# Performance work log

Hardware: AMD Instinct MI355X
Metric: run time of the kernel (lower is better)

The kernel has to match this reference:

```python
import jax, jax.numpy as jnp
import numpy as np

N, E, R = 30000, 300000, 3
IN, HID, OUT, HEADS = 256, 32, 64, 4
NEG_SLOPE = 0.2  # DGL GATConv default


def setup_inputs() -> dict:
    key = jax.random.key(0)
    ks = jax.random.split(key, 10)
    x = jax.random.normal(ks[0], (N, IN), jnp.float32)
    src = jax.random.randint(ks[1], (R, E), 0, N)
    dst = jax.random.randint(ks[2], (R, E), 0, N)
    s1 = (2.0 / IN) ** 0.5
    W1 = jax.random.normal(ks[3], (R, IN, HEADS * HID), jnp.float32) * s1
    attn_l1 = jax.random.normal(ks[4], (R, HEADS, HID), jnp.float32) * 0.1
    attn_r1 = jax.random.normal(ks[5], (R, HEADS, HID), jnp.float32) * 0.1
    b1 = jnp.zeros((R, HEADS * HID), jnp.float32)
    s2 = (2.0 / (HEADS * HID)) ** 0.5
    W2 = jax.random.normal(ks[6], (R, HEADS * HID, HEADS * OUT), jnp.float32) * s2
    attn_l2 = jax.random.normal(ks[7], (R, HEADS, OUT), jnp.float32) * 0.1
    attn_r2 = jax.random.normal(ks[8], (R, HEADS, OUT), jnp.float32) * 0.1
    b2 = jnp.zeros((R, HEADS * OUT), jnp.float32)
    return dict(x=x, src=src, dst=dst, W1=W1, attn_l1=attn_l1, attn_r1=attn_r1,
                b1=b1, W2=W2, attn_l2=attn_l2, attn_r2=attn_r2, b2=b2)


def _gat(x, s, d, W, al, ar, b):
    """Single-relation GATConv (DGL semantics): gather, edge softmax, scatter."""
    n = x.shape[0]
    H, D = al.shape
    z = (x @ W).reshape(n, H, D)                 # [n,H,D]
    el = (z * al[None]).sum(-1)                  # [n,H]
    er = (z * ar[None]).sum(-1)                  # [n,H]
    e = jax.nn.leaky_relu(el[s] + er[d], NEG_SLOPE)   # [E,H]
    m = jax.ops.segment_max(e, d, num_segments=n)     # stable edge softmax per dst
    w = jnp.exp(e - m[d])
    denom = jax.ops.segment_sum(w, d, num_segments=n)
    alpha = w / denom[d]                         # [E,H]
    out = jax.ops.segment_sum(alpha[:, :, None] * z[s], d, num_segments=n)  # [n,H,D]
    return out + b.reshape(1, H, D)


def reference(x, src, dst, W1, attn_l1, attn_r1, b1, W2, attn_l2, attn_r2, b2):
    gat_r = jax.vmap(_gat, in_axes=(None, 0, 0, 0, 0, 0, 0))
    # conv1: per-relation GAT summed across relations (HeteroGraphConv aggregate='sum')
    h = gat_r(x, src, dst, W1, attn_l1, attn_r1, b1).sum(0)      # [N,HEADS,HID]
    h = jax.nn.relu(h).reshape(-1, HEADS * HID)                  # [N,HEADS*HID]
    # conv2
    h2 = gat_r(h, src, dst, W2, attn_l2, attn_r2, b2).sum(0)     # [N,HEADS,OUT]
    return h2.mean(axis=1)                                       # [N,OUT]
```

## Files before the change

kernel.cpp:

```cpp
#include <hip/hip_runtime.h>
#include <math.h>

#define NNODES 30000
#define MPAD   30080
#define NEDGES 300000
#define NREL 3
#define IND 256
#define HIDD 32
#define OUTD 64
#define NHEADS 4
#define C1 (NHEADS*HIDD)
#define C2 (NHEADS*OUTD)
#define NEG_SLOPE 0.2f
#define CAP 64

typedef short bf16x8 __attribute__((ext_vector_type(8)));
typedef float f32x4  __attribute__((ext_vector_type(4)));
typedef float f32x2  __attribute__((ext_vector_type(2)));

__device__ __forceinline__ float b2f(unsigned short u) {
    return __uint_as_float(((unsigned)u) << 16);
}
__device__ __forceinline__ unsigned short f2b(float f) {
    unsigned u = __float_as_uint(f);
    u += 0x7fffu + ((u >> 16) & 1u);
    return (unsigned short)(u >> 16);
}

template<int CTRL>
__device__ __forceinline__ float dppadd(float x) {
    int s = __builtin_amdgcn_update_dpp(0, __float_as_int(x), CTRL, 0xf, 0xf, true);
    return x + __int_as_float(s);
}
__device__ __forceinline__ float dpp_wsum63(float x) {
    x = dppadd<0x111>(x);
    x = dppadd<0x112>(x);
    x = dppadd<0x114>(x);
    x = dppadd<0x118>(x);
    x = dppadd<0x142>(x);
    x = dppadd<0x143>(x);
    return x;
}
__device__ __forceinline__ float wave_rcp_sum(float w) {
    float den = __uint_as_float(__builtin_amdgcn_readlane(
        __float_as_uint(dpp_wsum63(w)), 63));
    return __builtin_amdgcn_rcpf(den);
}

template<int K, int N>
__device__ __forceinline__ void pack_w_dev(const float* __restrict__ W,
                                           unsigned short* __restrict__ P, int t) {
    const int KS = K / 32, NT = N / 16;
    int lane = t & 63;
    int fid = t >> 6;
    if (fid >= NREL * NT * KS) return;
    int ks = fid % KS;
    int nt = (fid / KS) % NT;
    int r  = fid / (KS * NT);
    int n  = nt * 16 + (lane & 15);
    int k0 = ks * 32 + (lane >> 4) * 8;
    const float* Wr = W + (size_t)r * K * N;
    unsigned short o[8];
#pragma unroll
    for (int j = 0; j < 8; j++) o[j] = f2b(Wr[(size_t)(k0 + j) * N + n]);
    unsigned short* dst = P + (size_t)fid * 512 + lane * 8;
    *(ushort4*)&dst[0] = *(ushort4*)&o[0];
    *(ushort4*)&dst[4] = *(ushort4*)&o[4];
}

__device__ __forceinline__ void pack_v_dev(const float* __restrict__ W2,
                                           unsigned short* __restrict__ P, int t) {
    const int KS = 16, NT = 4;
    int lane = t & 63;
    int fid = t >> 6;
    if (fid >= NREL * NT * KS) return;
    int ks = fid % KS;
    int nt = (fid / KS) % NT;
    int r  = fid / (KS * NT);
    int n  = nt * 16 + (lane & 15);
    int k0 = ks * 32 + (lane >> 4) * 8;
    const float* Wr = W2 + (size_t)r * C1 * C2;
    unsigned short o[8];
#pragma unroll
    for (int j = 0; j < 8; j++) {
        int k = k0 + j;
        int c = k & 127, h = k >> 7;
        o[j] = f2b(Wr[(size_t)c * C2 + h * OUTD + n]);
    }
    unsigned short* dst = P + (size_t)fid * 512 + lane * 8;
    *(ushort4*)&dst[0] = *(ushort4*)&o[0];
    *(ushort4*)&dst[4] = *(ushort4*)&o[4];
}

#define BF_BLOCKS ((NREL * NEDGES + 255) / 256)
#define PACK1_BLOCKS (NREL * (C1/16) * (IND/32) / 4)
#define PACKV_BLOCKS (NREL * 4 * 16 / 4)
#define VLR_BLOCKS 6
#define PREP_BLOCKS (BF_BLOCKS + PACK1_BLOCKS + PACKV_BLOCKS + VLR_BLOCKS + 1)
__global__ void prep_kernel(const int* __restrict__ src, const int* __restrict__ dst,
                            unsigned* __restrict__ cnt, int* __restrict__ buck,
                            const float* __restrict__ W1, unsigned short* __restrict__ P1,
                            const float* __restrict__ W2, unsigned short* __restrict__ PV,
                            const float* __restrict__ al2, const float* __restrict__ ar2,
                            const float* __restrict__ bb2,
                            float* __restrict__ tabs, float* __restrict__ biasout) {
    int b = blockIdx.x;
    if (b < BF_BLOCKS) {
        int gid = b * 256 + threadIdx.x;
        if (gid >= NREL * NEDGES) return;
        int r = gid / NEDGES;
        int d = dst[gid];
        int base = r * NNODES + d;
        unsigned pos = atomicAdd(&cnt[base], 1u);
        if (pos < CAP) buck[(size_t)base * CAP + pos] = src[gid];
    } else if (b < BF_BLOCKS + PACK1_BLOCKS) {
        pack_w_dev<IND, C1>(W1, P1, (b - BF_BLOCKS) * 256 + threadIdx.x);
    } else if (b < BF_BLOCKS + PACK1_BLOCKS + PACKV_BLOCKS) {
        pack_v_dev(W2, PV, (b - BF_BLOCKS - PACK1_BLOCKS) * 256 + threadIdx.x);
    } else if (b < BF_BLOCKS + PACK1_BLOCKS + PACKV_BLOCKS + VLR_BLOCKS) {
        int t = (b - BF_BLOCKS - PACK1_BLOCKS - PACKV_BLOCKS) * 256 + threadIdx.x;
        if (t < NREL * NHEADS * C1) {
            int c = t & 127, rh = t >> 7;
            const float* Wr = W2 + (size_t)(rh >> 2) * C1 * C2 + (size_t)c * C2 + (rh & 3) * OUTD;
            const float* alp = al2 + (size_t)rh * OUTD;
            const float* arp = ar2 + (size_t)rh * OUTD;
            float sl = 0.f, sr = 0.f;
#pragma unroll 4
            for (int d = 0; d < OUTD; d++) {
                sl = fmaf(Wr[d], alp[d], sl);
                sr = fmaf(Wr[d], arp[d], sr);
            }
            tabs[(rh * 2 + 0) * C1 + c] = sl;
            tabs[(rh * 2 + 1) * C1 + c] = sr;
        }
    } else {
        int t = threadIdx.x;
        if (t < OUTD) {
            float s = 0.f;
#pragma unroll
            for (int rh = 0; rh < NREL * NHEADS; rh++)
                s += bb2[(size_t)(rh >> 2) * C2 + (rh & 3) * OUTD + t];
            biasout[t] = 0.25f * s;
        }
    }
}

template<int K, int N>
__global__ __launch_bounds__(256) void mfma_gemm(
    const float* __restrict__ Ax, const unsigned short* __restrict__ Bp,
    const float* __restrict__ al, const float* __restrict__ ar,
    unsigned short* __restrict__ Zh, float* __restrict__ el, float* __restrict__ er)
{
    const int KS = K / 32, NT = N / 16, MT = 64, NP = N + 4;
    const int wave = threadIdx.x >> 6, lane = threadIdx.x & 63;
    const int r  = blockIdx.y;
    const int m0 = blockIdx.x * MT;
    const int fcol = lane & 15, quad = lane >> 4;

    __shared__ unsigned short zs[MT * (N + 4)];

    int m = m0 + wave * 16 + fcol;
    if (m >= NNODES) m = NNODES - 1;
    bf16x8 afrag[KS];
    const float* arowp = Ax + (size_t)m * K + quad * 8;
#pragma unroll
    for (int ks = 0; ks < KS; ks++) {
        float4 fa = *(const float4*)(arowp + ks * 32);
        float4 fb = *(const float4*)(arowp + ks * 32 + 4);
        unsigned short t[8] = { f2b(fa.x), f2b(fa.y), f2b(fa.z), f2b(fa.w),
                                f2b(fb.x), f2b(fb.y), f2b(fb.z), f2b(fb.w) };
        afrag[ks] = *(const bf16x8*)t;
    }

    f32x4 acc[NT];
#pragma unroll
    for (int nt = 0; nt < NT; nt++) { f32x4 z = {0.f,0.f,0.f,0.f}; acc[nt] = z; }

    const unsigned short* Bpr = Bp + (size_t)r * NT * KS * 512;
    for (int ks = 0; ks < KS; ks++) {
        bf16x8 b[NT];
#pragma unroll
        for (int nt = 0; nt < NT; nt++)
            b[nt] = *(const bf16x8*)(Bpr + ((size_t)nt * KS + ks) * 512 + lane * 8);
#pragma unroll
        for (int nt = 0; nt < NT; nt++)
            acc[nt] = __builtin_amdgcn_mfma_f32_16x16x32_bf16(afrag[ks], b[nt], acc[nt], 0, 0, 0);
    }

    {
        int lrow = wave * 16 + quad * 4;
#pragma unroll
        for (int nt = 0; nt < NT; nt++)
#pragma unroll
            for (int q = 0; q < 4; q++)
                zs[(lrow + q) * NP + nt * 16 + fcol] = f2b(acc[nt][q]);
    }
    __syncthreads();

    {
        uint2* zo = (uint2*)(Zh + ((size_t)r * MPAD + m0) * N);
        for (int i = threadIdx.x; i < MT * N / 4; i += 256) {
            int row = i / (N / 4), c4 = i % (N / 4);
            zo[i] = *(const uint2*)&zs[row * NP + c4 * 4];
        }
    }
    {
        const int D = N / NHEADS;
        int row = threadIdx.x >> 2, h = threadIdx.x & 3;
        int n = m0 + row;
        if (n < NNODES) {
            const float* alp = al + ((size_t)r * NHEADS + h) * D;
            const float* arp = ar + ((size_t)r * NHEADS + h) * D;
            const unsigned short* zp = zs + row * NP + h * D;
            float sl = 0.f, sr = 0.f;
#pragma unroll
            for (int d0 = 0; d0 < D; d0 += 4) {
                uint2 u = *(const uint2*)&zp[d0];
                float z0 = b2f((unsigned short)(u.x & 0xffff));
                float z1 = b2f((unsigned short)(u.x >> 16));
                float z2 = b2f((unsigned short)(u.y & 0xffff));
                float z3 = b2f((unsigned short)(u.y >> 16));
                sl = fmaf(z0, alp[d0], sl);     sr = fmaf(z0, arp[d0], sr);
                sl = fmaf(z1, alp[d0 + 1], sl); sr = fmaf(z1, arp[d0 + 1], sr);
                sl = fmaf(z2, alp[d0 + 2], sl); sr = fmaf(z2, arp[d0 + 2], sr);
                sl = fmaf(z3, alp[d0 + 3], sl); sr = fmaf(z3, arp[d0 + 3], sr);
            }
            el[((size_t)r * NNODES + n) * NHEADS + h] = sl;
            er[((size_t)r * NNODES + n) * NHEADS + h] = sr;
        }
    }
}

__global__ __launch_bounds__(256) void gat_gather1(
    const unsigned* __restrict__ cnt, const int* __restrict__ buck,
    const float* __restrict__ el, const float* __restrict__ er,
    const unsigned short* __restrict__ Zh, const float* __restrict__ b1,
    const float* __restrict__ tabs,
    unsigned short* __restrict__ hbh, float* __restrict__ el2, float* __restrict__ er2)
{
    __shared__ float atab[4][4 * 65];
    int wave = threadIdx.x >> 6, lane = threadIdx.x & 63;
    int n = blockIdx.x * 4 + wave;
    const int h0 = lane >> 4;
    float accx = 0.f, accy = 0.f;
    for (int r = 0; r < NREL; r++) {
        int base = r * NNODES + n;
        int c = (int)cnt[base]; c = c < CAP ? c : CAP;
        if (c == 0) continue;
        int s_all = buck[(size_t)base * CAP + (lane < c ? lane : c - 1)];
        float lg[4];
        if (lane < c) {
            const float4 e4 = *(const float4*)&el[((size_t)r * NNODES + s_all) * NHEADS];
            const float4 r4 = *(const float4*)&er[(size_t)base * NHEADS];
            float v;
            v = e4.x + r4.x; lg[0] = v > 0.f ? v : NEG_SLOPE * v;
            v = e4.y + r4.y; lg[1] = v > 0.f ? v : NEG_SLOPE * v;
            v = e4.z + r4.z; lg[2] = v > 0.f ? v : NEG_SLOPE * v;
            v = e4.w + r4.w; lg[3] = v > 0.f ? v : NEG_SLOPE * v;
        } else {
            lg[0] = lg[1] = lg[2] = lg[3] = -INFINITY;
        }
#pragma unroll
        for (int h = 0; h < 4; h++) {
            float w = __expf(lg[h]);
            float rinv = wave_rcp_sum(w);
            atab[wave][h * 65 + lane] = w * rinv;
        }
        const unsigned short* Zr = Zh + (size_t)r * MPAD * C1;
        const float* at = atab[wave] + h0 * 65;
        int cc = (c + 7) & ~7;
        for (int j = 0; j < cc; j += 8) {
            int ss[8];
#pragma unroll
            for (int q = 0; q < 8; q++) ss[q] = __builtin_amdgcn_readlane(s_all, j + q);
            unsigned zz[8];
#pragma unroll
            for (int q = 0; q < 8; q++)
                zz[q] = *(const unsigned*)&Zr[(size_t)ss[q] * C1 + 2 * lane];
#pragma unroll
            for (int q = 0; q < 8; q++) {
                float a0 = at[j + q];
                float z0 = __uint_as_float(zz[q] << 16);
                float z1 = __uint_as_float(zz[q] & 0xffff0000u);
                accx = fmaf(a0, z0, accx);
                accy = fmaf(a0, z1, accy);
            }
        }
    }
    int cch = 2 * lane;
    float bx = b1[cch]     + b1[C1 + cch]     + b1[2 * C1 + cch];
    float by = b1[cch + 1] + b1[C1 + cch + 1] + b1[2 * C1 + cch + 1];
    ushort2 o;
    o.x = f2b(fmaxf(accx + bx, 0.f));
    o.y = f2b(fmaxf(accy + by, 0.f));
    *(ushort2*)&hbh[(size_t)n * C1 + cch] = o;

    float hx = b2f(o.x), hy = b2f(o.y);
    for (int half = 0; half < 2; half++) {
        float p[12];
#pragma unroll
        for (int j = 0; j < 12; j++) {
            const float2 t = *(const float2*)&tabs[(half * 12 + j) * C1 + cch];
            p[j] = fmaf(hy, t.y, hx * t.x);
        }
#pragma unroll
        for (int j = 0; j < 12; j++) p[j] = dpp_wsum63(p[j]);
        if (lane == 63) {
#pragma unroll
            for (int j = 0; j < 12; j++) {
                int jj = half * 12 + j;
                int rh = jj >> 1;
                size_t idx = ((size_t)(rh >> 2) * NNODES + n) * NHEADS + (rh & 3);
                if (jj & 1) er2[idx] = p[j]; else el2[idx] = p[j];
            }
        }
    }
}

__global__ __launch_bounds__(512, 8) void gat_gather2f(
    const unsigned* __restrict__ cnt, const int* __restrict__ buck,
    const float* __restrict__ el, const float* __restrict__ er,
    const unsigned short* __restrict__ hbh, const unsigned short* __restrict__ PV,
    const float* __restrict__ biasout, float* __restrict__ out)
{
    __shared__ unsigned short aggs[8 * 1536];
    __shared__ float atv[8][64 * 4];
    const int wave = threadIdx.x >> 6, lane = threadIdx.x & 63;
    const int fcol = lane & 15, quad = lane >> 4;
    const int n0 = blockIdx.x * 8;
    const int n  = n0 + wave;

    for (int r = 0; r < NREL; r++) {
        f32x2 ag0 = {0.f, 0.f}, ag1 = {0.f, 0.f}, ag2 = {0.f, 0.f}, ag3 = {0.f, 0.f};

        int base = r * NNODES + n;
        int c = (int)cnt[base]; c = c < CAP ? c : CAP;
        if (c > 0) {
            int s_all = buck[(size_t)base * CAP + (lane < c ? lane : c - 1)];
            float lg[4];
            if (lane < c) {
                const float4 e4 = *(const float4*)&el[((size_t)r * NNODES + s_all) * NHEADS];
                const float4 r4 = *(const float4*)&er[(size_t)base * NHEADS];
                float v;
                v = e4.x + r4.x; lg[0] = v > 0.f ? v : NEG_SLOPE * v;
                v = e4.y + r4.y; lg[1] = v > 0.f ? v : NEG_SLOPE * v;
                v = e4.z + r4.z; lg[2] = v > 0.f ? v : NEG_SLOPE * v;
                v = e4.w + r4.w; lg[3] = v > 0.f ? v : NEG_SLOPE * v;
            } else {
                lg[0] = lg[1] = lg[2] = lg[3] = -INFINITY;
            }
            float aw[4];
#pragma unroll
            for (int h = 0; h < 4; h++) {
                float w = __expf(lg[h]);
                aw[h] = w * wave_rcp_sum(w);
            }
            float4 aq = { aw[0], aw[1], aw[2], aw[3] };
            *(float4*)&atv[wave][lane * 4] = aq;
            const float* at4 = &atv[wave][0];

            int cc = (c + 7) & ~7;
            for (int j = 0; j < cc; j += 8) {
                int ss[8];
#pragma unroll
                for (int q = 0; q < 8; q++) ss[q] = __builtin_amdgcn_readlane(s_all, j + q);
                unsigned zz[8];
#pragma unroll
                for (int q = 0; q < 8; q++)
                    zz[q] = *(const unsigned*)&hbh[(size_t)ss[q] * C1 + 2 * lane];
#pragma unroll
                for (int q = 0; q < 8; q++) {
                    f32x4 a4 = *(const f32x4*)&at4[(j + q) * 4];
                    f32x2 a01 = __builtin_shufflevector(a4, a4, 0, 1);
                    f32x2 a23 = __builtin_shufflevector(a4, a4, 2, 3);
                    f32x2 zp;
                    zp.x = __uint_as_float(zz[q] << 16);
                    zp.y = __uint_as_float(zz[q] & 0xffff0000u);
                    asm("v_pk_fma_f32 %0, %1, %2, %0 op_sel:[0,0,0] op_sel_hi:[0,1,1]"
                        : "+v"(ag0) : "v"(a01), "v"(zp));
                    asm("v_pk_fma_f32 %0, %1, %2, %0 op_sel:[1,0,0] op_sel_hi:[1,1,1]"
                        : "+v"(ag1) : "v"(a01), "v"(zp));
                    asm("v_pk_fma_f32 %0, %1, %2, %0 op_sel:[0,0,0] op_sel_hi:[0,1,1]"
                        : "+v"(ag2) : "v"(a23), "v"(zp));
                    asm("v_pk_fma_f32 %0, %1, %2, %0 op_sel:[1,0,0] op_sel_hi:[1,1,1]"
                        : "+v"(ag3) : "v"(a23), "v"(zp));
                }
            }
        }

        {
            unsigned sw = (unsigned)(wave << 4);
            char* basep = (char*)aggs + wave * 3072 + r * 1024;
            unsigned pk0 = ((unsigned)f2b(ag0.y) << 16) | f2b(ag0.x);
            unsigned pk1 = ((unsigned)f2b(ag1.y) << 16) | f2b(ag1.x);
            unsigned pk2 = ((unsigned)f2b(ag2.y) << 16) | f2b(ag2.x);
            unsigned pk3 = ((unsigned)f2b(ag3.y) << 16) | f2b(ag3.x);
            *(unsigned*)(basep + (((unsigned)(0 * 256 + lane * 4)) ^ sw)) = pk0;
            *(unsigned*)(basep + (((unsigned)(1 * 256 + lane * 4)) ^ sw)) = pk1;
            *(unsigned*)(basep + (((unsigned)(2 * 256 + lane * 4)) ^ sw)) = pk2;
            *(unsigned*)(basep + (((unsigned)(3 * 256 + lane * 4)) ^ sw)) = pk3;
        }
    }

    __syncthreads();

    if (wave < 4) {
        f32x4 acc = {0.f, 0.f, 0.f, 0.f};
        const int arow = fcol & 7;
        for (int rr = 0; rr < NREL; rr++) {
            const unsigned short* PVr = PV + ((size_t)(rr * 4 + wave) * 16) * 512;
#pragma unroll
            for (int ks = 0; ks < 16; ks++) {
                bf16x8 b = *(const bf16x8*)(PVr + (size_t)ks * 512 + lane * 8);
                const char* ap = (const char*)aggs + arow * 3072 +
                                 (((unsigned)(rr * 1024 + ks * 64 + quad * 16)) ^
                                  ((unsigned)(arow << 4)));
                bf16x8 a = *(const bf16x8*)ap;
                acc = __builtin_amdgcn_mfma_f32_16x16x32_bf16(a, b, acc, 0, 0, 0);
            }
        }
        if (quad < 2) {
            int col = wave * 16 + fcol;
            float bias = biasout[col];
#pragma unroll
            for (int q = 0; q < 4; q++) {
                int row = n0 + quad * 4 + q;
                out[(size_t)row * OUTD + col] = fmaf(0.25f, acc[q], bias);
            }
        }
    }
}

extern "C" void kernel_launch(void* const* d_in, const int* in_sizes, int n_in,
                              void* d_out, int out_size, void* d_ws, size_t ws_size,
                              hipStream_t stream) {
    (void)in_sizes; (void)n_in; (void)out_size; (void)ws_size;
    const float* x   = (const float*)d_in[0];
    const int*   src = (const int*)d_in[1];
    const int*   dst = (const int*)d_in[2];
    const float* W1  = (const float*)d_in[3];
    const float* al1 = (const float*)d_in[4];
    const float* ar1 = (const float*)d_in[5];
    const float* b1  = (const float*)d_in[6];
    const float* W2  = (const float*)d_in[7];
    const float* al2 = (const float*)d_in[8];
    const float* ar2 = (const float*)d_in[9];
    const float* b2  = (const float*)d_in[10];
    float* out = (float*)d_out;

    float* ws = (float*)d_ws;
    size_t off = 0;
    unsigned short* Zh  = (unsigned short*)(ws + off); off += (size_t)NREL * MPAD * C1 / 2;
    unsigned short* hbh = (unsigned short*)(ws + off); off += (size_t)NNODES * C1 / 2;
    unsigned short* P1  = (unsigned short*)(ws + off); off += (size_t)NREL * (C1/16) * (IND/32) * 512 / 2;
    unsigned short* PV  = (unsigned short*)(ws + off); off += (size_t)NREL * 4 * 16 * 512 / 2;
    float* el  = ws + off; off += (size_t)NREL * NNODES * NHEADS;
    float* er  = ws + off; off += (size_t)NREL * NNODES * NHEADS;
    float* el2 = ws + off; off += (size_t)NREL * NNODES * NHEADS;
    float* er2 = ws + off; off += (size_t)NREL * NNODES * NHEADS;
    unsigned* cnt = (unsigned*)(ws + off); off += (size_t)NREL * NNODES;
    int* buck  = (int*)(ws + off); off += (size_t)NREL * NNODES * CAP;
    float* tabs    = ws + off; off += 24 * C1;
    float* biasout = ws + off; off += OUTD;

    const int TB = 256;

    hipMemsetAsync(cnt, 0, (size_t)NREL * NNODES * sizeof(unsigned), stream);
    prep_kernel<<<PREP_BLOCKS, TB, 0, stream>>>(src, dst, cnt, buck,
                                                W1, P1, W2, PV, al2, ar2, b2,
                                                tabs, biasout);

    {
        dim3 grid(MPAD / 64, NREL);
        mfma_gemm<IND, C1><<<grid, 256, 0, stream>>>(x, P1, al1, ar1, Zh, el, er);
    }
    gat_gather1<<<NNODES / 4, 256, 0, stream>>>(cnt, buck, el, er, Zh, b1, tabs,
                                                hbh, el2, er2);

    gat_gather2f<<<NNODES / 8, 512, 0, stream>>>(cnt, buck, el2, er2, hbh, PV, biasout, out);
}
```

Before: 301.1 us.

## Defer softmax normalization and prefetch next relation's bucket indices in gather kernels

Both gather kernels now store unnormalized exp weights and apply the reciprocal of the wave-summed denominator after the weighted accumulation, so the DPP reduction and readlane no longer sit on the critical path before the feature gathers. The next relation's edge count and source indices are loaded one iteration early so their latency overlaps the current relation's gather loop. The attention table stride changes to 68 so it can be read with float4 loads. This adds register pressure and changes rounding slightly because normalization now happens after accumulation.

Result: no change. 302.5 us (+0.5%).

```diff
diff --git a/kernel.cpp b/kernel.cpp
--- a/kernel.cpp
+++ b/kernel.cpp
@@ -41,10 +41,8 @@
     x = dppadd<0x143>(x);
     return x;
 }
-__device__ __forceinline__ float wave_rcp_sum(float w) {
-    float den = __uint_as_float(__builtin_amdgcn_readlane(
-        __float_as_uint(dpp_wsum63(w)), 63));
-    return __builtin_amdgcn_rcpf(den);
+__device__ __forceinline__ float rl63f(float x) {
+    return __uint_as_float(__builtin_amdgcn_readlane(__float_as_uint(x), 63));
 }
 
 template<int K, int N>
@@ -238,54 +236,82 @@
     const float* __restrict__ tabs,
     unsigned short* __restrict__ hbh, float* __restrict__ el2, float* __restrict__ er2)
 {
-    __shared__ float atab[4][4 * 65];
+    __shared__ float atab[4][4 * 68];
     int wave = threadIdx.x >> 6, lane = threadIdx.x & 63;
     int n = blockIdx.x * 4 + wave;
     const int h0 = lane >> 4;
     float accx = 0.f, accy = 0.f;
+
+    int c = (int)cnt[n]; c = c < CAP ? c : CAP;
+    int sidx0 = lane < c ? lane : c - 1; if (sidx0 < 0) sidx0 = 0;
+    int s_all = buck[(size_t)n * CAP + sidx0];
+
+#pragma unroll
     for (int r = 0; r < NREL; r++) {
         int base = r * NNODES + n;
-        int c = (int)cnt[base]; c = c < CAP ? c : CAP;
-        if (c == 0) continue;
-        int s_all = buck[(size_t)base * CAP + (lane < c ? lane : c - 1)];
-        float lg[4];
-        if (lane < c) {
-            const float4 e4 = *(const float4*)&el[((size_t)r * NNODES + s_all) * NHEADS];
-            const float4 r4 = *(const float4*)&er[(size_t)base * NHEADS];
-            float v;
-            v = e4.x + r4.x; lg[0] = v > 0.f ? v : NEG_SLOPE * v;
-            v = e4.y + r4.y; lg[1] = v > 0.f ? v : NEG_SLOPE * v;
-            v = e4.z + r4.z; lg[2] = v > 0.f ? v : NEG_SLOPE * v;
-            v = e4.w + r4.w; lg[3] = v > 0.f ? v : NEG_SLOPE * v;
-        } else {
-            lg[0] = lg[1] = lg[2] = lg[3] = -INFINITY;
-        }
-#pragma unroll
-        for (int h = 0; h < 4; h++) {
-            float w = __expf(lg[h]);
-            float rinv = wave_rcp_sum(w);
-            atab[wave][h * 65 + lane] = w * rinv;
-        }
-        const unsigned short* Zr = Zh + (size_t)r * MPAD * C1;
-        const float* at = atab[wave] + h0 * 65;
-        int cc = (c + 7) & ~7;
-        for (int j = 0; j < cc; j += 8) {
-            int ss[8];
-#pragma unroll
-            for (int q = 0; q < 8; q++) ss[q] = __builtin_amdgcn_readlane(s_all, j + q);
-            unsigned zz[8];
-#pragma unroll
-            for (int q = 0; q < 8; q++)
-                zz[q] = *(const unsigned*)&Zr[(size_t)ss[q] * C1 + 2 * lane];
-#pragma unroll
-            for (int q = 0; q < 8; q++) {
-                float a0 = at[j + q];
-                float z0 = __uint_as_float(zz[q] << 16);
-                float z1 = __uint_as_float(zz[q] & 0xffff0000u);
-                accx = fmaf(a0, z0, accx);
-                accy = fmaf(a0, z1, accy);
-            }
-        }
+        int cn = 0;
+        if (r + 1 < NREL) {
+            cn = (int)cnt[base + NNODES]; cn = cn < CAP ? cn : CAP;
+        }
+        float d0 = 0.f, d1 = 0.f, d2 = 0.f, d3 = 0.f;
+        if (c > 0) {
+            float lg[4];
+            if (lane < c) {
+                const float4 e4 = *(const float4*)&el[((size_t)r * NNODES + s_all) * NHEADS];
+                const float4 r4 = *(const float4*)&er[(size_t)base * NHEADS];
+                float v;
+                v = e4.x + r4.x; lg[0] = v > 0.f ? v : NEG_SLOPE * v;
+                v = e4.y + r4.y; lg[1] = v > 0.f ? v : NEG_SLOPE * v;
+                v = e4.z + r4.z; lg[2] = v > 0.f ? v : NEG_SLOPE * v;
+                v = e4.w + r4.w; lg[3] = v > 0.f ? v : NEG_SLOPE * v;
+            } else {
+                lg[0] = lg[1] = lg[2] = lg[3] = -INFINITY;
+            }
+            float w0 = __expf(lg[0]), w1 = __expf(lg[1]);
+            float w2 = __expf(lg[2]), w3 = __expf(lg[3]);
+            atab[wave][0 * 68 + lane] = w0;
+            atab[wave][1 * 68 + lane] = w1;
+            atab[wave][2 * 68 + lane] = w2;
+            atab[wave][3 * 68 + lane] = w3;
+            d0 = dpp_wsum63(w0); d1 = dpp_wsum63(w1);
+            d2 = dpp_wsum63(w2); d3 = dpp_wsum63(w3);
+        }
+        int sn = 0;
+        if (r + 1 < NREL) {
+            int sidxn = lane < cn ? lane : cn - 1; if (sidxn < 0) sidxn = 0;
+            sn = buck[(size_t)(base + NNODES) * CAP + sidxn];
+        }
+        if (c > 0) {
+            const unsigned short* Zr = Zh + (size_t)r * MPAD * C1;
+            const float* at = atab[wave] + h0 * 68;
+            float px = 0.f, py = 0.f;
+            int cc = (c + 7) & ~7;
+            for (int j = 0; j < cc; j += 8) {
+                int ss[8];
+#pragma unroll
+                for (int q = 0; q < 8; q++) ss[q] = __builtin_amdgcn_readlane(s_all, j + q);
+                unsigned zz[8];
+#pragma unroll
+                for (int q = 0; q < 8; q++)
+                    zz[q] = *(const unsigned*)&Zr[(size_t)ss[q] * C1 + 2 * lane];
+                float4 aA = *(const float4*)&at[j];
+                float4 aB = *(const float4*)&at[j + 4];
+                float av[8] = { aA.x, aA.y, aA.z, aA.w, aB.x, aB.y, aB.z, aB.w };
+#pragma unroll
+                for (int q = 0; q < 8; q++) {
+                    float z0 = __uint_as_float(zz[q] << 16);
+                    float z1 = __uint_as_float(zz[q] & 0xffff0000u);
+                    px = fmaf(av[q], z0, px);
+                    py = fmaf(av[q], z1, py);
+                }
+            }
+            float dn0 = rl63f(d0), dn1 = rl63f(d1), dn2 = rl63f(d2), dn3 = rl63f(d3);
+            float den = h0 == 0 ? dn0 : h0 == 1 ? dn1 : h0 == 2 ? dn2 : dn3;
+            float rinv = __builtin_amdgcn_rcpf(den);
+            accx = fmaf(rinv, px, accx);
+            accy = fmaf(rinv, py, accy);
+        }
+        c = cn; s_all = sn;
     }
     int cch = 2 * lane;
     float bx = b1[cch]     + b1[C1 + cch]     + b1[2 * C1 + cch];
@@ -330,13 +356,20 @@
     const int n0 = blockIdx.x * 8;
     const int n  = n0 + wave;
 
+    int c = (int)cnt[n]; c = c < CAP ? c : CAP;
+    int sidx0 = lane < c ? lane : c - 1; if (sidx0 < 0) sidx0 = 0;
+    int s_all = buck[(size_t)n * CAP + sidx0];
+
+#pragma unroll
     for (int r = 0; r < NREL; r++) {
+        int base = r * NNODES + n;
+        int cn = 0;
+        if (r + 1 < NREL) {
+            cn = (int)cnt[base + NNODES]; cn = cn < CAP ? cn : CAP;
+        }
         f32x2 ag0 = {0.f, 0.f}, ag1 = {0.f, 0.f}, ag2 = {0.f, 0.f}, ag3 = {0.f, 0.f};
-
-        int base = r * NNODES + n;
-        int c = (int)cnt[base]; c = c < CAP ? c : CAP;
+        float d0 = 0.f, d1 = 0.f, d2 = 0.f, d3 = 0.f;
         if (c > 0) {
-            int s_all = buck[(size_t)base * CAP + (lane < c ? lane : c - 1)];
             float lg[4];
             if (lane < c) {
                 const float4 e4 = *(const float4*)&el[((size_t)r * NNODES + s_all) * NHEADS];
@@ -349,16 +382,20 @@
             } else {
                 lg[0] = lg[1] = lg[2] = lg[3] = -INFINITY;
             }
-            float aw[4];
-#pragma unroll
-            for (int h = 0; h < 4; h++) {
-                float w = __expf(lg[h]);
-                aw[h] = w * wave_rcp_sum(w);
-            }
-            float4 aq = { aw[0], aw[1], aw[2], aw[3] };
+            float w0 = __expf(lg[0]), w1 = __expf(lg[1]);
+            float w2 = __expf(lg[2]), w3 = __expf(lg[3]);
+            float4 aq = { w0, w1, w2, w3 };
             *(float4*)&atv[wave][lane * 4] = aq;
+            d0 = dpp_wsum63(w0); d1 = dpp_wsum63(w1);
+            d2 = dpp_wsum63(w2); d3 = dpp_wsum63(w3);
+        }
+        int sn = 0;
+        if (r + 1 < NREL) {
+            int sidxn = lane < cn ? lane : cn - 1; if (sidxn < 0) sidxn = 0;
+            sn = buck[(size_t)(base + NNODES) * CAP + sidxn];
+        }
+        if (c > 0) {
             const float* at4 = &atv[wave][0];
-
             int cc = (c + 7) & ~7;
             for (int j = 0; j < cc; j += 8) {
                 int ss[8];
@@ -386,6 +423,12 @@
                         : "+v"(ag3) : "v"(a23), "v"(zp));
                 }
             }
+            float r0 = __builtin_amdgcn_rcpf(rl63f(d0));
+            float r1 = __builtin_amdgcn_rcpf(rl63f(d1));
+            float r2 = __builtin_amdgcn_rcpf(rl63f(d2));
+            float r3 = __builtin_amdgcn_rcpf(rl63f(d3));
+            ag0.x *= r0; ag0.y *= r0;  ag1.x *= r1; ag1.y *= r1;
+            ag2.x *= r2; ag2.y *= r2;  ag3.x *= r3; ag3.y *= r3;
         }
 
         {
@@ -400,6 +443,7 @@
             *(unsigned*)(basep + (((unsigned)(2 * 256 + lane * 4)) ^ sw)) = pk2;
             *(unsigned*)(basep + (((unsigned)(3 * 256 + lane * 4)) ^ sw)) = pk3;
         }
+        c = cn; s_all = sn;
     }
 
     __syncthreads();
```
